# Kernel optimization log

Measured on AMD Instinct MI355X. Metric: run time of the kernel, lower is better.

The kernel has to match this reference:

```python
import jax, jax.numpy as jnp
import numpy as np

B, T, H = 4, 4096, 2048
G_EPS = 0.5
LN_EPS = 1e-5
INIT_STD = 0.02


def setup_inputs() -> dict:
    key = jax.random.key(0)
    ks = jax.random.split(key, 4)
    return {
        "hidden_states": jax.random.normal(ks[0], (B, T, H), jnp.float32),
        "W_z": jax.random.normal(ks[1], (H, H), jnp.float32) * INIT_STD,
        "b_z": jnp.zeros((H,), jnp.float32),
        "W_h": jax.random.normal(ks[2], (H, H), jnp.float32) * INIT_STD,
        "b_h": jnp.zeros((H,), jnp.float32),
        "ln_w": jnp.ones((H,), jnp.float32),
        "ln_b": jnp.zeros((H,), jnp.float32),
        "h0": jax.random.normal(ks[3], (H,), jnp.float32) * INIT_STD,
    }


def _g_log(x):
    # torch.where(x >= 0, log(relu(x) + g_eps), -softplus(-x))
    return jnp.where(x >= 0, jnp.log(jax.nn.relu(x) + G_EPS), -jax.nn.softplus(-x))


def reference(hidden_states, W_z, b_z, W_h, b_h, ln_w, ln_b, h0):
    Bc, Tc, Hc = hidden_states.shape
    k = hidden_states @ W_z.T + b_z                      # [B,T,H]
    log_z = -jax.nn.softplus(-k)                         # log sigmoid(k)
    log_coeffs = -jax.nn.softplus(k)                     # log(1 - sigmoid(k))
    log_tilde_h = _g_log(hidden_states @ W_h.T + b_h)    # [B,T,H]
    log_h0 = jnp.broadcast_to(_g_log(h0), (Bc, 1, Hc))
    log_values = jnp.concatenate([log_h0, log_z + log_tilde_h], axis=1)  # [B,T+1,H]
    # NOTE: faithful to source: cumsum over the LAST (hidden) dim, then pad one
    # zero row at the front of the time dim (F.pad(..., (0,0,1,0))).
    a_star = jnp.pad(jnp.cumsum(log_coeffs, axis=-1), ((0, 0), (1, 0), (0, 0)))  # [B,T+1,H]
    log_h = a_star + jax.lax.cumlogsumexp(log_values - a_star, axis=1)
    # global mean / unbiased std normalization, as in source
    log_h = (log_h - log_h.mean()) / jnp.std(log_h, ddof=1)
    h = jnp.exp(log_h)[:, 1:, :]                         # drop the h0 step
    # residual + LayerNorm (dropout is identity in eval)
    x = h + hidden_states
    mu = x.mean(axis=-1, keepdims=True)
    var = x.var(axis=-1, keepdims=True)
    return (x - mu) * jax.lax.rsqrt(var + LN_EPS) * ln_w + ln_b
```

## Files before the change

### kernel.cpp

```cpp
#include <hip/hip_runtime.h>
#include <stdint.h>

constexpr int NB = 4;
constexpr int NT = 4096;
constexpr int NH = 2048;
constexpr int MROWS = NB * NT;
constexpr int TP1 = NT + 1;
constexpr int CH2 = 17;
constexpr int NCH2 = 241;
constexpr int GSZ = 16;
constexpr int NGRP = (NCH2 + GSZ - 1) / GSZ;
constexpr int NCOL = NB * NH;

typedef unsigned short u16;
typedef __bf16 bf16x8 __attribute__((ext_vector_type(8)));
typedef float f32x4 __attribute__((ext_vector_type(4)));
typedef unsigned short u16x8 __attribute__((ext_vector_type(8)));
typedef _Float16 h16x8 __attribute__((ext_vector_type(8)));
typedef u16x8 __attribute__((may_alias)) u16x8_a;
typedef h16x8 __attribute__((may_alias)) h16x8_a;
typedef float4 __attribute__((may_alias)) float4_a;

__device__ __forceinline__ u16 f2bf(float f) {
  unsigned int u = __float_as_uint(f);
  return (u16)((u + 0x7fffu + ((u >> 16) & 1u)) >> 16);
}
__device__ __forceinline__ float bf2f(u16 v) {
  return __uint_as_float(((unsigned int)v) << 16);
}
__device__ __forceinline__ float spf_(float x) {
  return fmaxf(x, 0.f) + __logf(1.f + __expf(-fabsf(x)));
}
__device__ __forceinline__ float glogf_(float x) {
  return (x >= 0.f) ? __logf(x + 0.5f) : -spf_(-x);
}
__device__ __forceinline__ void gld16(const void* g, void* l) {
  __builtin_amdgcn_global_load_lds((const __attribute__((address_space(1))) void*)g,
                                   (__attribute__((address_space(3))) void*)l, 16, 0, 0);
}
__device__ __forceinline__ void ld8(const float* p, float* r) {
  float4 a = *(const float4_a*)p, b = *(const float4_a*)(p + 4);
  r[0] = a.x; r[1] = a.y; r[2] = a.z; r[3] = a.w;
  r[4] = b.x; r[5] = b.y; r[6] = b.z; r[7] = b.w;
}
__device__ __forceinline__ void st8(float* p, const float* r) {
  *(float4_a*)p       = make_float4(r[0], r[1], r[2], r[3]);
  *(float4_a*)(p + 4) = make_float4(r[4], r[5], r[6], r[7]);
}
__device__ __forceinline__ void lsecomb(float& M, float& S, float Mo, float So) {
  const float Mn = fmaxf(M, Mo);
  float Sn = S * __expf(M - Mn) + So * __expf(Mo - Mn);
  if (Mn == -INFINITY) Sn = 0.f;
  M = Mn; S = Sn;
}

__global__ __launch_bounds__(256) void cvt_all(
    const float* __restrict__ hs, const float* __restrict__ Wz,
    const float* __restrict__ Wh, u16* __restrict__ hsb,
    u16* __restrict__ wzb, u16* __restrict__ whb) {
  const int s0 = MROWS * NH / 8;
  const int s1 = s0 + NH * NH / 8;
  const int s2 = s1 + NH * NH / 8;
  int i = blockIdx.x * 256 + threadIdx.x;
  if (i >= s2) return;
  const float* in; u16* out; int j;
  if (i < s0)      { in = hs; out = hsb; j = i; }
  else if (i < s1) { in = Wz; out = wzb; j = i - s0; }
  else             { in = Wh; out = whb; j = i - s1; }
  const float4* p = (const float4*)in;
  float4 a = p[2 * (size_t)j], b = p[2 * (size_t)j + 1];
  u16x8 o;
  o[0] = f2bf(a.x); o[1] = f2bf(a.y); o[2] = f2bf(a.z); o[3] = f2bf(a.w);
  o[4] = f2bf(b.x); o[5] = f2bf(b.y); o[6] = f2bf(b.z); o[7] = f2bf(b.w);
  *(u16x8*)(out + (size_t)j * 8) = o;
}

__global__ __launch_bounds__(256, 3) void gemm_bt(
    const u16* __restrict__ A,
    const u16* __restrict__ Bz, const u16* __restrict__ Bh,
    const float* __restrict__ bz, const float* __restrict__ bh,
    u16* __restrict__ KU) {
  const u16* Bm  = blockIdx.y ? Bh : Bz;
  const float* bias = blockIdx.y ? bh : bz;
  u16* Cw = KU + (blockIdx.y ? 2048 : 0);

  const int bid = blockIdx.x;
  const int wg = (bid & 7) * 256 + (bid >> 3);
  const int bx = wg & 15;
  const int by = wg >> 4;
  const int row0 = by << 7, col0 = bx << 7;

  __shared__ u16 ldsA[128 * 64];
  __shared__ u16 ldsB[128 * 64];

  const int tid = threadIdx.x;
  const int lane = tid & 63;
  const int wv = tid >> 6;
  const int wr = (wv >> 1) << 6;
  const int wc = (wv & 1) << 6;

  const int srow = lane >> 3;
  const int sslot = ((lane & 7) ^ srow) << 3;
  const int xsw = (lane & 7) << 3;
  const int q8 = (lane >> 4) << 3;
  const int f15 = lane & 15;

  f32x4 acc[4][4] = {};

  for (int k0 = 0; k0 < NH; k0 += 64) {
    if (k0) __syncthreads();
#pragma unroll
    for (int i = 0; i < 4; ++i) {
      const int r = i * 32 + wv * 8 + srow;
      const size_t gcol = (size_t)(k0 + sslot);
      gld16(A  + (size_t)(row0 + r) * NH + gcol, &ldsA[(size_t)(i * 256 + wv * 64) * 8]);
      gld16(Bm + (size_t)(col0 + r) * NH + gcol, &ldsB[(size_t)(i * 256 + wv * 64) * 8]);
    }
    __syncthreads();
#pragma unroll
    for (int ks = 0; ks < 2; ++ks) {
      const int cphys = ((ks << 5) | q8) ^ xsw;
      bf16x8 af[4], bfr[4];
#pragma unroll
      for (int m = 0; m < 4; ++m)
        af[m] = *(const bf16x8*)&ldsA[(wr + m * 16 + f15) * 64 + cphys];
#pragma unroll
      for (int n = 0; n < 4; ++n)
        bfr[n] = *(const bf16x8*)&ldsB[(wc + n * 16 + f15) * 64 + cphys];
#pragma unroll
      for (int m = 0; m < 4; ++m)
#pragma unroll
        for (int n = 0; n < 4; ++n)
          acc[m][n] = __builtin_amdgcn_mfma_f32_16x16x32_bf16(af[m], bfr[n], acc[m][n], 0, 0, 0);
    }
  }

  const int fr = lane & 15, fq = lane >> 4;
#pragma unroll
  for (int n = 0; n < 4; ++n) {
    const int col = col0 + wc + n * 16 + fr;
    const float bv = bias[col];
#pragma unroll
    for (int m = 0; m < 4; ++m) {
#pragma unroll
      for (int v = 0; v < 4; ++v) {
        const int row = row0 + wr + m * 16 + fq * 4 + v;
        Cw[(size_t)row * 4096 + col] = f2bf(acc[m][n][v] + bv);
      }
    }
  }
}

__device__ __forceinline__ void row_pointwise(const char* KU, size_t row,
                                              int tid, float* lc, float* lv) {
  const size_t rb = row * 8192;
  u16x8 kv = *(const u16x8_a*)(KU + rb + tid * 16);
  u16x8 uv = *(const u16x8_a*)(KU + rb + 4096 + tid * 16);
#pragma unroll
  for (int e = 0; e < 8; ++e) {
    const float k = bf2f(kv[e]);
    const float L = __logf(1.f + __expf(-fabsf(k)));
    lc[e] = -fmaxf(k, 0.f) - L;
    lv[e] = fminf(k, 0.f) - L + glogf_(bf2f(uv[e]));
  }
}

__global__ __launch_bounds__(256) void carry_pass(
    const char* __restrict__ KU, float* __restrict__ cm, float* __restrict__ cs,
    const float* __restrict__ h0) {
  const int ch = blockIdx.x;
  const int b = blockIdx.y;
  const int tid = threadIdx.x;
  const int lane = tid & 63, wvx = tid >> 6;
  const int t0 = ch * CH2;
  const int t1 = (t0 + CH2 < TP1) ? (t0 + CH2) : TP1;

  float m8[8], s8[8];
#pragma unroll
  for (int e = 0; e < 8; ++e) { m8[e] = -INFINITY; s8[e] = 0.f; }

  __shared__ float wsum[2][4];

  float lc[8], lv[8];
  {
    const int tf = (t0 < 1) ? 1 : t0;
    if (tf < t1) row_pointwise(KU, (size_t)b * NT + (tf - 1), tid, lc, lv);
  }

  for (int tt = t0; tt < t1; ++tt) {
    if (tt == 0) {
#pragma unroll
      for (int e = 0; e < 8; ++e) {
        const float x = glogf_(h0[tid * 8 + e]);
        m8[e] = x; s8[e] = 1.f;
      }
      continue;
    }
    float nlc[8], nlv[8];
    const bool pf = (tt + 1 < t1);
    if (pf) row_pointwise(KU, (size_t)b * NT + tt, tid, nlc, nlv);

    float cum[8], run = 0.f;
#pragma unroll
    for (int e = 0; e < 8; ++e) { run += lc[e]; cum[e] = run; }
    float v = run;
#pragma unroll
    for (int d = 1; d < 64; d <<= 1) {
      float o = __shfl_up(v, d, 64);
      if (lane >= d) v += o;
    }
    const int par = tt & 1;
    if (lane == 63) wsum[par][wvx] = v;
    __syncthreads();
    float base = v - run;
#pragma unroll
    for (int w = 0; w < 4; ++w)
      if (w < wvx) base += wsum[par][w];

#pragma unroll
    for (int e = 0; e < 8; ++e) {
      const float x = lv[e] - (base + cum[e]);
      const float nm = fmaxf(m8[e], x);
      s8[e] = s8[e] * __expf(m8[e] - nm) + __expf(x - nm);
      m8[e] = nm;
    }
    if (pf) {
#pragma unroll
      for (int e = 0; e < 8; ++e) { lc[e] = nlc[e]; lv[e] = nlv[e]; }
    }
  }
  const size_t co = ((size_t)ch * NB + b) * NH + tid * 8;
  st8(cm + co, m8);
  st8(cs + co, s8);
}

__global__ __launch_bounds__(256) void carry_groupred(
    const float* __restrict__ cm, const float* __restrict__ cs,
    float* __restrict__ gm, float* __restrict__ gs) {
  const int c = blockIdx.x * 256 + threadIdx.x;
  const int g = blockIdx.y;
  const int ch0 = g * GSZ;
  const int ch1 = (ch0 + GSZ < NCH2) ? (ch0 + GSZ) : NCH2;
  float M = -INFINITY, S = 0.f;
  for (int ch = ch0; ch < ch1; ++ch) {
    const size_t o = (size_t)ch * NCOL + c;
    lsecomb(M, S, cm[o], cs[o]);
  }
  gm[(size_t)g * NCOL + c] = M;
  gs[(size_t)g * NCOL + c] = S;
}

__global__ __launch_bounds__(256) void carry_groupscan(float* __restrict__ gm,
                                                       float* __restrict__ gs) {
  const int c = blockIdx.x * 256 + threadIdx.x;
  float M = -INFINITY, S = 0.f;
  for (int g = 0; g < NGRP; ++g) {
    const size_t o = (size_t)g * NCOL + c;
    const float m2 = gm[o], s2 = gs[o];
    gm[o] = M; gs[o] = S;
    lsecomb(M, S, m2, s2);
  }
}

__global__ __launch_bounds__(256) void carry_apply(
    float* __restrict__ cm, float* __restrict__ cs,
    const float* __restrict__ gm, const float* __restrict__ gs) {
  const int c = blockIdx.x * 256 + threadIdx.x;
  const int g = blockIdx.y;
  const int ch0 = g * GSZ;
  const int ch1 = (ch0 + GSZ < NCH2) ? (ch0 + GSZ) : NCH2;
  float M = gm[(size_t)g * NCOL + c];
  float S = gs[(size_t)g * NCOL + c];
  for (int ch = ch0; ch < ch1; ++ch) {
    const size_t o = (size_t)ch * NCOL + c;
    const float m2 = cm[o], s2 = cs[o];
    cm[o] = M; cs[o] = S;
    lsecomb(M, S, m2, s2);
  }
}

template <int HLH>
__global__ __launch_bounds__(256) void scan_final(
    const char* __restrict__ KU, float* __restrict__ LH32,
    _Float16* __restrict__ LH16,
    const float* __restrict__ cm, const float* __restrict__ cs,
    const float* __restrict__ h0, double* __restrict__ sums) {
  const int ch = blockIdx.x;
  const int b = blockIdx.y;
  const int tid = threadIdx.x;
  const int lane = tid & 63, wvx = tid >> 6;
  const int t0 = ch * CH2;
  const int t1 = (t0 + CH2 < TP1) ? (t0 + CH2) : TP1;

  float m8[8], s8[8];
  {
    const size_t co = ((size_t)ch * NB + b) * NH + tid * 8;
    ld8(cm + co, m8);
    ld8(cs + co, s8);
  }

  __shared__ float wsum[2][4];
  double s1 = 0.0, s2 = 0.0;

  float lc[8], lv[8];
  {
    const int tf = (t0 < 1) ? 1 : t0;
    if (tf < t1) row_pointwise(KU, (size_t)b * NT + (tf - 1), tid, lc, lv);
  }

  for (int tt = t0; tt < t1; ++tt) {
    if (tt == 0) {
#pragma unroll
      for (int e = 0; e < 8; ++e) {
        const float x = glogf_(h0[tid * 8 + e]);
        m8[e] = x; s8[e] = 1.f;
        s1 += (double)x;
        s2 += (double)x * (double)x;
      }
      continue;
    }
    float nlc[8], nlv[8];
    const bool pf = (tt + 1 < t1);
    if (pf) row_pointwise(KU, (size_t)b * NT + tt, tid, nlc, nlv);

    float cum[8], run = 0.f;
#pragma unroll
    for (int e = 0; e < 8; ++e) { run += lc[e]; cum[e] = run; }
    float v = run;
#pragma unroll
    for (int d = 1; d < 64; d <<= 1) {
      float o = __shfl_up(v, d, 64);
      if (lane >= d) v += o;
    }
    const int par = tt & 1;
    if (lane == 63) wsum[par][wvx] = v;
    __syncthreads();
    float base = v - run;
#pragma unroll
    for (int w = 0; w < 4; ++w)
      if (w < wvx) base += wsum[par][w];

    float lh8[8];
#pragma unroll
    for (int e = 0; e < 8; ++e) {
      const float as = base + cum[e];
      const float x = lv[e] - as;
      const float nm = fmaxf(m8[e], x);
      s8[e] = s8[e] * __expf(m8[e] - nm) + __expf(x - nm);
      m8[e] = nm;
      const float lh = as + nm + __logf(s8[e]);
      lh8[e] = lh;
      s1 += (double)lh;
      s2 += (double)lh * (double)lh;
    }
    const size_t row = (size_t)b * NT + (tt - 1);
    if (HLH) {
      h16x8 hv;
#pragma unroll
      for (int e = 0; e < 8; ++e) hv[e] = (_Float16)lh8[e];
      *(h16x8_a*)(LH16 + row * NH + tid * 8) = hv;
    } else {
      st8(LH32 + row * NH + tid * 8, lh8);
    }
    if (pf) {
#pragma unroll
      for (int e = 0; e < 8; ++e) { lc[e] = nlc[e]; lv[e] = nlv[e]; }
    }
  }
  double v1 = s1, v2 = s2;
#pragma unroll
  for (int d = 32; d; d >>= 1) {
    v1 += __shfl_down(v1, d, 64);
    v2 += __shfl_down(v2, d, 64);
  }
  __shared__ double dr1[4], dr2[4];
  if (lane == 0) { dr1[wvx] = v1; dr2[wvx] = v2; }
  __syncthreads();
  if (tid == 0) {
    atomicAdd(&sums[0], dr1[0] + dr1[1] + dr1[2] + dr1[3]);
    atomicAdd(&sums[1], dr2[0] + dr2[1] + dr2[2] + dr2[3]);
  }
}

__global__ void finalize_stats(const double* __restrict__ sums,
                               float* __restrict__ stats) {
  const double S = sums[0], S2 = sums[1];
  const double N = (double)NB * (double)TP1 * (double)NH;
  const double mu = S / N;
  const double var = (S2 - S * S / N) / (N - 1.0);
  stats[0] = (float)mu;
  stats[1] = (float)(1.0 / sqrt(var));
}

template <int HLH>
__global__ __launch_bounds__(256) void final_ln(
    float* __restrict__ OUT, const float* __restrict__ LH32,
    const _Float16* __restrict__ LH16, const u16* __restrict__ hsb,
    const float* __restrict__ lnw, const float* __restrict__ lnb,
    const float* __restrict__ stats) {
  const int tid = threadIdx.x;
  const size_t off = (size_t)blockIdx.x * NH + tid * 8;
  const float mu_g = stats[0], isd = stats[1];

  float lh[8], av[8];
  if (HLH) {
    h16x8 hv = *(const h16x8_a*)(LH16 + off);
#pragma unroll
    for (int e = 0; e < 8; ++e) lh[e] = (float)hv[e];
  } else {
    ld8(LH32 + off, lh);
  }
  {
    u16x8 hv = *(const u16x8_a*)(hsb + off);
#pragma unroll
    for (int e = 0; e < 8; ++e) av[e] = bf2f(hv[e]);
  }
  float x[8];
  float s = 0.f, q = 0.f;
#pragma unroll
  for (int e = 0; e < 8; ++e) {
    x[e] = __expf((lh[e] - mu_g) * isd) + av[e];
    s += x[e];
    q += x[e] * x[e];
  }
#pragma unroll
  for (int d = 32; d; d >>= 1) {
    s += __shfl_down(s, d, 64);
    q += __shfl_down(q, d, 64);
  }
  __shared__ float r1[4], r2[4];
  const int lane = tid & 63, wvx = tid >> 6;
  if (lane == 0) { r1[wvx] = s; r2[wvx] = q; }
  __syncthreads();
  const float st = r1[0] + r1[1] + r1[2] + r1[3];
  const float qt = r2[0] + r2[1] + r2[2] + r2[3];
  const float mean = st * (1.0f / NH);
  const float var = qt * (1.0f / NH) - mean * mean;
  const float rstd = rsqrtf(var + 1e-5f);

  float wv8[8], bv8[8];
  ld8(lnw + tid * 8, wv8);
  ld8(lnb + tid * 8, bv8);
  float o[8];
#pragma unroll
  for (int e = 0; e < 8; ++e)
    o[e] = (x[e] - mean) * rstd * wv8[e] + bv8[e];
  st8(OUT + off, o);
}

extern "C" void kernel_launch(void* const* d_in, const int* in_sizes, int n_in,
                              void* d_out, int out_size, void* d_ws, size_t ws_size,
                              hipStream_t stream) {
  (void)in_sizes; (void)n_in; (void)out_size;
  const float* hs  = (const float*)d_in[0];
  const float* Wz  = (const float*)d_in[1];
  const float* bz  = (const float*)d_in[2];
  const float* Wh  = (const float*)d_in[3];
  const float* bh  = (const float*)d_in[4];
  const float* lnw = (const float*)d_in[5];
  const float* lnb = (const float*)d_in[6];
  const float* h0  = (const float*)d_in[7];
  float* out = (float*)d_out;

  char* w0 = (char*)d_ws;
  char* w = w0;
  u16* hsb   = (u16*)w;  w += (size_t)MROWS * NH * 2;
  u16* wzb   = (u16*)w;  w += (size_t)NH * NH * 2;
  u16* whb   = (u16*)w;  w += (size_t)NH * NH * 2;
  char* KU   = w;        w += (size_t)MROWS * 8192;
  double* sums = (double*)w; w += 16;
  float* stats = (float*)w;  w += 64;
  float* gm_ = (float*)w;    w += (size_t)NGRP * NCOL * 4;
  float* gs_ = (float*)w;    w += (size_t)NGRP * NCOL * 4;
  _Float16* LH16 = (_Float16*)w;
  const size_t need_half = (size_t)(w - w0) + (size_t)MROWS * NH * 2;
  const bool use_half = (ws_size >= need_half);
  float* cm_ = (float*)wzb;
  float* cs_ = cm_ + (size_t)NCH2 * NCOL;

  hipMemsetAsync(sums, 0, 16, stream);

  {
    const int tot8 = MROWS * NH / 8 + 2 * (NH * NH / 8);
    cvt_all<<<dim3((tot8 + 255) / 256), 256, 0, stream>>>(hs, Wz, Wh, hsb, wzb, whb);
  }

  gemm_bt<<<dim3((MROWS / 128) * (NH / 128), 2), 256, 0, stream>>>(
      hsb, wzb, whb, bz, bh, (u16*)KU);

  carry_pass<<<dim3(NCH2, NB), 256, 0, stream>>>(KU, cm_, cs_, h0);

  carry_groupred<<<dim3(NCOL / 256, NGRP), 256, 0, stream>>>(cm_, cs_, gm_, gs_);
  carry_groupscan<<<dim3(NCOL / 256), 256, 0, stream>>>(gm_, gs_);
  carry_apply<<<dim3(NCOL / 256, NGRP), 256, 0, stream>>>(cm_, cs_, gm_, gs_);

  if (use_half)
    scan_final<1><<<dim3(NCH2, NB), 256, 0, stream>>>(KU, out, LH16, cm_, cs_, h0, sums);
  else
    scan_final<0><<<dim3(NCH2, NB), 256, 0, stream>>>(KU, out, LH16, cm_, cs_, h0, sums);
  finalize_stats<<<1, 1, 0, stream>>>(sums, stats);

  if (use_half)
    final_ln<1><<<dim3(MROWS), 256, 0, stream>>>(out, out, LH16, hsb, lnw, lnb, stats);
  else
    final_ln<0><<<dim3(MROWS), 256, 0, stream>>>(out, out, LH16, hsb, lnw, lnb, stats);
}
```

Measured before the change: 554.5 us.

## Fuse softplus/g_log pointwise into GEMM epilogue and store fp16 log terms

The GEMM epilogue now computes the log-coefficient, log-sigmoid and g_log terms and stores them as fp16 in a three-plane row buffer. Both scan passes then only load and add, instead of recomputing the transcendentals per element twice. scan_final writes log_h in place into the first plane of that buffer, which removes the separate LH buffer and the workspace-size fallback. In exchange the GEMM epilogue does more scattered 2-byte stores, per-row traffic grows from 8 KB to 12 KB, and the fp16 intermediates lose precision.

Result: no change. 561.1 us (+1.2%).

```diff
diff --git a/kernel.cpp b/kernel.cpp
--- a/kernel.cpp
+++ b/kernel.cpp
@@ -11,6 +11,7 @@
 constexpr int GSZ = 16;
 constexpr int NGRP = (NCH2 + GSZ - 1) / GSZ;
 constexpr int NCOL = NB * NH;
+constexpr int RBYTES = 12288;
 
 typedef unsigned short u16;
 typedef __bf16 bf16x8 __attribute__((ext_vector_type(8)));
@@ -79,10 +80,9 @@
     const u16* __restrict__ A,
     const u16* __restrict__ Bz, const u16* __restrict__ Bh,
     const float* __restrict__ bz, const float* __restrict__ bh,
-    u16* __restrict__ KU) {
+    char* __restrict__ KU) {
   const u16* Bm  = blockIdx.y ? Bh : Bz;
   const float* bias = blockIdx.y ? bh : bz;
-  u16* Cw = KU + (blockIdx.y ? 2048 : 0);
 
   const int bid = blockIdx.x;
   const int wg = (bid & 7) * 256 + (bid >> 3);
@@ -136,32 +136,53 @@
   }
 
   const int fr = lane & 15, fq = lane >> 4;
-#pragma unroll
-  for (int n = 0; n < 4; ++n) {
-    const int col = col0 + wc + n * 16 + fr;
-    const float bv = bias[col];
-#pragma unroll
-    for (int m = 0; m < 4; ++m) {
-#pragma unroll
-      for (int v = 0; v < 4; ++v) {
-        const int row = row0 + wr + m * 16 + fq * 4 + v;
-        Cw[(size_t)row * 4096 + col] = f2bf(acc[m][n][v] + bv);
+  if (blockIdx.y == 0) {
+#pragma unroll
+    for (int n = 0; n < 4; ++n) {
+      const int col = col0 + wc + n * 16 + fr;
+      const float bv = bias[col];
+#pragma unroll
+      for (int m = 0; m < 4; ++m) {
+#pragma unroll
+        for (int v = 0; v < 4; ++v) {
+          const int row = row0 + wr + m * 16 + fq * 4 + v;
+          const float k = acc[m][n][v] + bv;
+          const float L = __logf(1.f + __expf(-fabsf(k)));
+          _Float16* rp = (_Float16*)(KU + (size_t)row * RBYTES);
+          rp[col]        = (_Float16)(-fmaxf(k, 0.f) - L);
+          rp[col + 2048] = (_Float16)(fminf(k, 0.f) - L);
+        }
       }
     }
-  }
-}
-
-__device__ __forceinline__ void row_pointwise(const char* KU, size_t row,
-                                              int tid, float* lc, float* lv) {
-  const size_t rb = row * 8192;
-  u16x8 kv = *(const u16x8_a*)(KU + rb + tid * 16);
-  u16x8 uv = *(const u16x8_a*)(KU + rb + 4096 + tid * 16);
+  } else {
+#pragma unroll
+    for (int n = 0; n < 4; ++n) {
+      const int col = col0 + wc + n * 16 + fr;
+      const float bv = bias[col];
+#pragma unroll
+      for (int m = 0; m < 4; ++m) {
+#pragma unroll
+        for (int v = 0; v < 4; ++v) {
+          const int row = row0 + wr + m * 16 + fq * 4 + v;
+          const float u = acc[m][n][v] + bv;
+          _Float16* rp = (_Float16*)(KU + (size_t)row * RBYTES);
+          rp[col + 4096] = (_Float16)glogf_(u);
+        }
+      }
+    }
+  }
+}
+
+__device__ __forceinline__ void row_load(const char* KU, size_t row,
+                                         int tid, float* lc, float* lv) {
+  const char* rb = KU + row * RBYTES;
+  h16x8 c = *(const h16x8_a*)(rb + tid * 16);
+  h16x8 s = *(const h16x8_a*)(rb + 4096 + tid * 16);
+  h16x8 g = *(const h16x8_a*)(rb + 8192 + tid * 16);
 #pragma unroll
   for (int e = 0; e < 8; ++e) {
-    const float k = bf2f(kv[e]);
-    const float L = __logf(1.f + __expf(-fabsf(k)));
-    lc[e] = -fmaxf(k, 0.f) - L;
-    lv[e] = fminf(k, 0.f) - L + glogf_(bf2f(uv[e]));
+    lc[e] = (float)c[e];
+    lv[e] = (float)s[e] + (float)g[e];
   }
 }
 
@@ -184,7 +205,7 @@
   float lc[8], lv[8];
   {
     const int tf = (t0 < 1) ? 1 : t0;
-    if (tf < t1) row_pointwise(KU, (size_t)b * NT + (tf - 1), tid, lc, lv);
+    if (tf < t1) row_load(KU, (size_t)b * NT + (tf - 1), tid, lc, lv);
   }
 
   for (int tt = t0; tt < t1; ++tt) {
@@ -198,7 +219,7 @@
     }
     float nlc[8], nlv[8];
     const bool pf = (tt + 1 < t1);
-    if (pf) row_pointwise(KU, (size_t)b * NT + tt, tid, nlc, nlv);
+    if (pf) row_load(KU, (size_t)b * NT + tt, tid, nlc, nlv);
 
     float cum[8], run = 0.f;
 #pragma unroll
@@ -279,10 +300,8 @@
   }
 }
 
-template <int HLH>
 __global__ __launch_bounds__(256) void scan_final(
-    const char* __restrict__ KU, float* __restrict__ LH32,
-    _Float16* __restrict__ LH16,
+    char* __restrict__ KU,
     const float* __restrict__ cm, const float* __restrict__ cs,
     const float* __restrict__ h0, double* __restrict__ sums) {
   const int ch = blockIdx.x;
@@ -305,7 +324,7 @@
   float lc[8], lv[8];
   {
     const int tf = (t0 < 1) ? 1 : t0;
-    if (tf < t1) row_pointwise(KU, (size_t)b * NT + (tf - 1), tid, lc, lv);
+    if (tf < t1) row_load(KU, (size_t)b * NT + (tf - 1), tid, lc, lv);
   }
 
   for (int tt = t0; tt < t1; ++tt) {
@@ -321,7 +340,7 @@
     }
     float nlc[8], nlv[8];
     const bool pf = (tt + 1 < t1);
-    if (pf) row_pointwise(KU, (size_t)b * NT + tt, tid, nlc, nlv);
+    if (pf) row_load(KU, (size_t)b * NT + tt, tid, nlc, nlv);
 
     float cum[8], run = 0.f;
 #pragma unroll
@@ -340,7 +359,7 @@
     for (int w = 0; w < 4; ++w)
       if (w < wvx) base += wsum[par][w];
 
-    float lh8[8];
+    h16x8 lhv;
 #pragma unroll
     for (int e = 0; e < 8; ++e) {
       const float as = base + cum[e];
@@ -349,19 +368,12 @@
       s8[e] = s8[e] * __expf(m8[e] - nm) + __expf(x - nm);
       m8[e] = nm;
       const float lh = as + nm + __logf(s8[e]);
-      lh8[e] = lh;
+      lhv[e] = (_Float16)lh;
       s1 += (double)lh;
       s2 += (double)lh * (double)lh;
     }
     const size_t row = (size_t)b * NT + (tt - 1);
-    if (HLH) {
-      h16x8 hv;
-#pragma unroll
-      for (int e = 0; e < 8; ++e) hv[e] = (_Float16)lh8[e];
-      *(h16x8_a*)(LH16 + row * NH + tid * 8) = hv;
-    } else {
-      st8(LH32 + row * NH + tid * 8, lh8);
-    }
+    *(h16x8_a*)(KU + row * RBYTES + tid * 16) = lhv;
     if (pf) {
 #pragma unroll
       for (int e = 0; e < 8; ++e) { lc[e] = nlc[e]; lv[e] = nlv[e]; }
@@ -392,23 +404,21 @@
   stats[1] = (float)(1.0 / sqrt(var));
 }
 
-template <int HLH>
 __global__ __launch_bounds__(256) void final_ln(
-    float* __restrict__ OUT, const float* __restrict__ LH32,
-    const _Float16* __restrict__ LH16, const u16* __restrict__ hsb,
+    float* __restrict__ OUT, const char* __restrict__ KU,
+    const u16* __restrict__ hsb,
     const float* __restrict__ lnw, const float* __restrict__ lnb,
     const float* __restrict__ stats) {
   const int tid = threadIdx.x;
-  const size_t off = (size_t)blockIdx.x * NH + tid * 8;
+  const size_t row = blockIdx.x;
+  const size_t off = row * NH + tid * 8;
   const float mu_g = stats[0], isd = stats[1];
 
   float lh[8], av[8];
-  if (HLH) {
-    h16x8 hv = *(const h16x8_a*)(LH16 + off);
+  {
+    h16x8 hv = *(const h16x8_a*)(KU + row * RBYTES + tid * 16);
 #pragma unroll
     for (int e = 0; e < 8; ++e) lh[e] = (float)hv[e];
-  } else {
-    ld8(LH32 + off, lh);
   }
   {
     u16x8 hv = *(const u16x8_a*)(hsb + off);
@@ -451,7 +461,7 @@
 extern "C" void kernel_launch(void* const* d_in, const int* in_sizes, int n_in,
                               void* d_out, int out_size, void* d_ws, size_t ws_size,
                               hipStream_t stream) {
-  (void)in_sizes; (void)n_in; (void)out_size;
+  (void)in_sizes; (void)n_in; (void)out_size; (void)ws_size;
   const float* hs  = (const float*)d_in[0];
   const float* Wz  = (const float*)d_in[1];
   const float* bz  = (const float*)d_in[2];
@@ -462,19 +472,15 @@
   const float* h0  = (const float*)d_in[7];
   float* out = (float*)d_out;
 
-  char* w0 = (char*)d_ws;
-  char* w = w0;
+  char* w = (char*)d_ws;
   u16* hsb   = (u16*)w;  w += (size_t)MROWS * NH * 2;
   u16* wzb   = (u16*)w;  w += (size_t)NH * NH * 2;
   u16* whb   = (u16*)w;  w += (size_t)NH * NH * 2;
-  char* KU   = w;        w += (size_t)MROWS * 8192;
+  char* KU   = w;        w += (size_t)MROWS * RBYTES;
   double* sums = (double*)w; w += 16;
   float* stats = (float*)w;  w += 64;
   float* gm_ = (float*)w;    w += (size_t)NGRP * NCOL * 4;
   float* gs_ = (float*)w;    w += (size_t)NGRP * NCOL * 4;
-  _Float16* LH16 = (_Float16*)w;
-  const size_t need_half = (size_t)(w - w0) + (size_t)MROWS * NH * 2;
-  const bool use_half = (ws_size >= need_half);
   float* cm_ = (float*)wzb;
   float* cs_ = cm_ + (size_t)NCH2 * NCOL;
 
@@ -486,7 +492,7 @@
   }
 
   gemm_bt<<<dim3((MROWS / 128) * (NH / 128), 2), 256, 0, stream>>>(
-      hsb, wzb, whb, bz, bh, (u16*)KU);
+      hsb, wzb, whb, bz, bh, KU);
 
   carry_pass<<<dim3(NCH2, NB), 256, 0, stream>>>(KU, cm_, cs_, h0);
 
@@ -494,14 +500,8 @@
   carry_groupscan<<<dim3(NCOL / 256), 256, 0, stream>>>(gm_, gs_);
   carry_apply<<<dim3(NCOL / 256, NGRP), 256, 0, stream>>>(cm_, cs_, gm_, gs_);
 
-  if (use_half)
-    scan_final<1><<<dim3(NCH2, NB), 256, 0, stream>>>(KU, out, LH16, cm_, cs_, h0, sums);
-  else
-    scan_final<0><<<dim3(NCH2, NB), 256, 0, stream>>>(KU, out, LH16, cm_, cs_, h0, sums);
+  scan_final<<<dim3(NCH2, NB), 256, 0, stream>>>(KU, cm_, cs_, h0, sums);
   finalize_stats<<<1, 1, 0, stream>>>(sums, stats);
 
-  if (use_half)
-    final_ln<1><<<dim3(MROWS), 256, 0, stream>>>(out, out, LH16, hsb, lnw, lnb, stats);
-  else
-    final_ln<0><<<dim3(MROWS), 256, 0, stream>>>(out, out, LH16, hsb, lnw, lnb, stats);
-}
+  final_ln<<<dim3(MROWS), 256, 0, stream>>>(out, KU, hsb, lnw, lnb, stats);
+}
```
